# Kernel tuning notes

Hardware: AMD Instinct MI355X
Metric: run time of the kernel (lower is better)

The kernel has to match this reference:

```python
import jax, jax.numpy as jnp
import numpy as np

E = 4        # num_edge_types
C = 4        # num_channels (must equal E due to module's layer>0 einsum)
N = 2048     # num_nodes
W_IN = 256
W_OUT = 128


def _xavier_uniform(key, shape):
    # torch.nn.init.xavier_uniform_ on a 2D tensor [fan_out, fan_in] style
    fan_out, fan_in = shape[0], shape[1]
    bound = float(np.sqrt(6.0 / (fan_in + fan_out)))
    return jax.random.uniform(key, shape, jnp.float32, -bound, bound)


def setup_inputs() -> dict:
    key = jax.random.key(0)
    k = jax.random.split(key, 7)
    A = jax.random.uniform(k[0], (E, N, N), jnp.float32)   # non-negative dense multi-relation adjacency
    X = jax.random.normal(k[1], (N, W_IN), jnp.float32)
    gt_w1 = _xavier_uniform(k[2], (C, E))   # layer0 conv1
    gt_w2 = _xavier_uniform(k[3], (C, E))   # layer0 conv2
    gt_w3 = _xavier_uniform(k[4], (C, C))   # layer1 conv1 (C == E)
    gcn_w = _xavier_uniform(k[5], (W_IN, W_OUT))
    gcn_b = jnp.zeros((W_OUT,), jnp.float32)
    return {"A": A, "X": X, "gt_w1": gt_w1, "gt_w2": gt_w2, "gt_w3": gt_w3,
            "gcn_w": gcn_w, "gcn_b": gcn_b}


def _normalize_adj(adj):
    # adj: [N, N]. Symmetric degree normalization D^-1/2 (A+I) D^-1/2,
    # expressed as broadcasted row/col scaling (math-identical to the
    # original diag-matmul-matmul formulation).
    adj = adj + jnp.eye(adj.shape[0], dtype=adj.dtype)
    deg = adj.sum(axis=1)
    d = deg ** -0.5
    d = jnp.where(jnp.isinf(d), jnp.zeros_like(d), d)
    return d[:, None] * adj * d[None, :]


def reference(A, X, gt_w1, gt_w2, gt_w3, gcn_w, gcn_b):
    # --- GT layer 0 (first=True): two softmax-weighted mixes of A, then bmm ---
    fw1 = jax.nn.softmax(gt_w1, axis=1)
    fw2 = jax.nn.softmax(gt_w2, axis=1)
    Ha = jnp.einsum('oi,inm->onm', fw1, A)   # [C, N, N]
    Hb = jnp.einsum('oi,inm->onm', fw2, A)   # [C, N, N]
    H = jnp.matmul(Ha, Hb)                   # [C, N, N]
    # --- GT layer 1 (first=False): H @ (softmax mix of A) ---
    fw3 = jax.nn.softmax(gt_w3, axis=1)
    Hc = jnp.einsum('oi,inm->onm', fw3, A)   # [C, N, N]
    H = jnp.matmul(H, Hc)                    # [C, N, N]
    # --- per-channel degree-normalized GCN conv ---
    Hn = jax.vmap(_normalize_adj)(H)         # [C, N, N]
    support = X @ gcn_w                      # [N, W_OUT] (shared across channels)
    out = jnp.einsum('cnm,mf->cnf', Hn, support) + gcn_b  # [C, N, W_OUT]
    out = jax.nn.relu(out)
    # torch.cat(X_out, dim=1): channel blocks side by side -> [N, C*W_OUT]
    return jnp.transpose(out, (1, 0, 2)).reshape(N, C * W_OUT)
```

## Files before the change

kernel.cpp:

```cpp
#include <hip/hip_runtime.h>
#include <math.h>

#define N_NODES 2048
#define NNE ((long)N_NODES * N_NODES)

#define SUPD_SCALE 8192.0f

typedef _Float16 half4_t __attribute__((ext_vector_type(4)));
typedef _Float16 half8_t __attribute__((ext_vector_type(8)));
typedef float    floatx4 __attribute__((ext_vector_type(4)));

__device__ __forceinline__ void async_cp16(const void* g, void* l) {
  __builtin_amdgcn_global_load_lds((const __attribute__((address_space(1))) void*)g,
                                   (__attribute__((address_space(3))) void*)l,
                                   16, 0, 0);
}

__device__ __forceinline__ float colscale_from(float cn) {
  return exp2f((float)(10 - ilogbf(fmaxf(cn, 1e-37f))));
}

__global__ void softmax3_zero_k(const float* __restrict__ w1,
                                const float* __restrict__ w2,
                                const float* __restrict__ w3,
                                float* __restrict__ fw,
                                float* __restrict__ cn) {
  int t = threadIdx.x;
  float4 z4 = {0.f, 0.f, 0.f, 0.f};
  ((float4*)cn)[t] = z4;
  if (t < 12) {
    const float* src = (t < 4) ? w1 : (t < 8) ? w2 : w3;
    int r = t & 3;
    float v0 = src[r * 4 + 0], v1 = src[r * 4 + 1];
    float v2 = src[r * 4 + 2], v3 = src[r * 4 + 3];
    float m = fmaxf(fmaxf(v0, v1), fmaxf(v2, v3));
    float e0 = expf(v0 - m), e1 = expf(v1 - m), e2 = expf(v2 - m), e3 = expf(v3 - m);
    float inv = 1.0f / (e0 + e1 + e2 + e3);
    fw[t * 4 + 0] = e0 * inv; fw[t * 4 + 1] = e1 * inv;
    fw[t * 4 + 2] = e2 * inv; fw[t * 4 + 3] = e3 * inv;
  }
}

__global__ __launch_bounds__(128)
void support_k(const float* __restrict__ X, const float* __restrict__ W,
               float* __restrict__ sup) {
  __shared__ float Xs[256];
  const int t = threadIdx.x;
  const int m = blockIdx.x;
  Xs[t]       = X[(long)m * 256 + t];
  Xs[t + 128] = X[(long)m * 256 + t + 128];
  __syncthreads();
  float acc = 0.f;
  #pragma unroll 8
  for (int k = 0; k < 256; ++k) acc = fmaf(Xs[k], W[(long)k * 128 + t], acc);
  sup[(long)m * 128 + t] = acc;
}

__global__ __launch_bounds__(256)
void rc_from_A_k(const float* __restrict__ A, const float* __restrict__ fw,
                 float* __restrict__ rc) {
  __shared__ float red[4][4];
  const int r = blockIdx.x;
  const int w = threadIdx.x >> 6, lane = threadIdx.x & 63;
  float se[4];
  #pragma unroll
  for (int e = 0; e < 4; ++e) {
    const float4* row = (const float4*)(A + (long)e * NNE + (long)r * N_NODES);
    float s = 0.f;
    #pragma unroll
    for (int q = 0; q < 2; ++q) {
      float4 a = row[w * 128 + q * 64 + lane];
      s += (a.x + a.y) + (a.z + a.w);
    }
    se[e] = s;
  }
  float m[4];
  #pragma unroll
  for (int c = 0; c < 4; ++c)
    m[c] = fw[32 + c * 4 + 0] * se[0] + fw[32 + c * 4 + 1] * se[1] +
           fw[32 + c * 4 + 2] * se[2] + fw[32 + c * 4 + 3] * se[3];
  #pragma unroll
  for (int o = 32; o > 0; o >>= 1) {
    #pragma unroll
    for (int c = 0; c < 4; ++c) m[c] += __shfl_down(m[c], o, 64);
  }
  if (lane == 0) {
    #pragma unroll
    for (int c = 0; c < 4; ++c) red[w][c] = m[c];
  }
  __syncthreads();
  if (threadIdx.x < 4) {
    int c = threadIdx.x;
    rc[c * N_NODES + r] = (red[0][c] + red[1][c]) + (red[2][c] + red[3][c]);
  }
}

__global__ __launch_bounds__(256)
void matvecA_k(const float* __restrict__ A, const float* __restrict__ fw, int off,
               const float* __restrict__ vin, float* __restrict__ vout) {
  __shared__ float red[4][4];
  const int r = blockIdx.x;
  const int w = threadIdx.x >> 6, lane = threadIdx.x & 63;
  float acc[4][4] = {{0.f}};
  #pragma unroll
  for (int q = 0; q < 2; ++q) {
    const int j4 = w * 128 + q * 64 + lane;
    float4 v0 = *(const float4*)&vin[0 * 2048 + j4 * 4];
    float4 v1 = *(const float4*)&vin[1 * 2048 + j4 * 4];
    float4 v2 = *(const float4*)&vin[2 * 2048 + j4 * 4];
    float4 v3 = *(const float4*)&vin[3 * 2048 + j4 * 4];
    #pragma unroll
    for (int e = 0; e < 4; ++e) {
      float4 a = *(const float4*)(A + (long)e * NNE + (long)r * N_NODES + j4 * 4);
      acc[e][0] += (a.x * v0.x + a.y * v0.y) + (a.z * v0.z + a.w * v0.w);
      acc[e][1] += (a.x * v1.x + a.y * v1.y) + (a.z * v1.z + a.w * v1.w);
      acc[e][2] += (a.x * v2.x + a.y * v2.y) + (a.z * v2.z + a.w * v2.w);
      acc[e][3] += (a.x * v3.x + a.y * v3.y) + (a.z * v3.z + a.w * v3.w);
    }
  }
  float m[4];
  #pragma unroll
  for (int c = 0; c < 4; ++c)
    m[c] = fw[off + c * 4 + 0] * acc[0][c] + fw[off + c * 4 + 1] * acc[1][c] +
           fw[off + c * 4 + 2] * acc[2][c] + fw[off + c * 4 + 3] * acc[3][c];
  #pragma unroll
  for (int o = 32; o > 0; o >>= 1) {
    #pragma unroll
    for (int c = 0; c < 4; ++c) m[c] += __shfl_down(m[c], o, 64);
  }
  if (lane == 0) {
    #pragma unroll
    for (int c = 0; c < 4; ++c) red[w][c] = m[c];
  }
  __syncthreads();
  if (threadIdx.x < 4) {
    int c = threadIdx.x;
    vout[c * N_NODES + r] = (red[0][c] + red[1][c]) + (red[2][c] + red[3][c]);
  }
}

__global__ __launch_bounds__(256)
void transposeV_k(const float* __restrict__ sup, const float* __restrict__ deg,
                  float* __restrict__ dvec,
                  _Float16* __restrict__ TH, _Float16* __restrict__ TL,
                  float* __restrict__ cn0) {
  __shared__ _Float16 sh[32][33], sl[32][33];
  __shared__ float red[8][32];
  const int t = threadIdx.x;
  const int z = blockIdx.z;
  const int m0 = blockIdx.x * 32, f0 = blockIdx.y * 32;
  const int r0 = t >> 5, col = t & 31;
  float part = 0.f;
  #pragma unroll
  for (int m = 0; m < 4; ++m) {
    const int row = m0 + r0 + 8 * m;
    float dm = 1.0f / sqrtf(1.0f + deg[(long)z * N_NODES + row]);
    float sv = sup[(long)row * 128 + f0 + col] * dm;
    if (blockIdx.y == 0 && col == 0) dvec[(long)z * N_NODES + row] = dm;
    float v = sv * SUPD_SCALE;
    _Float16 h = (_Float16)v;
    sh[r0 + 8 * m][col] = h;
    sl[r0 + 8 * m][col] = (_Float16)(v - (float)h);
    part += fabsf(v);
  }
  red[r0][col] = part;
  __syncthreads();
  if (t < 32) {
    float s = 0.f;
    #pragma unroll
    for (int q = 0; q < 8; ++q) s += red[q][t];
    atomicAdd(&cn0[(long)z * 128 + f0 + t], s);
  }
  const int rr = t >> 3, cq = (t & 7) * 4;
  half4_t oh, ol;
  #pragma unroll
  for (int d = 0; d < 4; ++d) { oh[d] = sh[cq + d][rr]; ol[d] = sl[cq + d][rr]; }
  long ob = (long)z * 128 * N_NODES + (long)(f0 + rr) * N_NODES + m0 + cq;
  *(half4_t*)(TH + ob) = oh;
  *(half4_t*)(TL + ob) = ol;
}

__global__ __launch_bounds__(256, 2)
void gemm_mix_k(const float* __restrict__ A, const float* __restrict__ fw, int off,
                const _Float16* __restrict__ BH, const _Float16* __restrict__ BL,
                float* __restrict__ C) {
  __shared__ __align__(16) _Float16 BsArr[3 * 8192];
  __shared__ __align__(16) _Float16 HsArr[2 * 2048];

  const int t = threadIdx.x;
  const int lane = t & 63;
  const int w = t >> 6;
  const int bid = blockIdx.x;
  const int tile = bid & 63;
  const int ch = (bid >> 6) & 3;
  const int kc = bid >> 8;
  const int i0 = tile * 32;
  const long koff = (long)kc * 512;

  float wv[4];
  #pragma unroll
  for (int e = 0; e < 4; ++e) wv[e] = fw[off + ch * 4 + e];

  const int rr = t >> 3;
  const int k4 = (t & 7) * 4;
  const float* gA = A + (long)(i0 + rr) * N_NODES + koff + k4;
  const int hoff = rr * 32 + (((k4 >> 3) + (rr >> 1)) & 3) * 8 + (k4 & 7);

  const int hls = w >> 1;
  const int half = w & 1;
  const int kc_st = (((lane & 3) - ((lane >> 3) & 3)) & 3) * 8;
  const _Float16* gB = (hls ? BL : BH)
                     + ((long)ch * 128 + half * 64 + (lane >> 2)) * (long)N_NODES
                     + koff + kc_st;

  const int wm = w >> 1, wn = w & 1;
  const int fr = lane & 15;
  const int fq = lane >> 4;
  const int fkz = ((fq + (fr >> 1)) & 3) * 8;
  const int aoff = (wm * 16 + fr) * 32 + fkz;

  floatx4 acc[4];
  #pragma unroll
  for (int j = 0; j < 4; ++j) {
    floatx4 zz4 = {0.f, 0.f, 0.f, 0.f};
    acc[j] = zz4;
  }

  float4 sA[4], sB[4], sC[4];

  auto loadA = [&](float4* av, int kt) {
    const float* g = gA + kt * 32;
    av[0] = *(const float4*)(g);
    av[1] = *(const float4*)(g + NNE);
    av[2] = *(const float4*)(g + 2 * NNE);
    av[3] = *(const float4*)(g + 3 * NNE);
  };
  auto stageB = [&](int buf, int kt) {
    _Float16* lb = BsArr + buf * 8192 + hls * 4096 + half * 2048;
    const _Float16* g = gB + kt * 32;
    #pragma unroll
    for (int q = 0; q < 4; ++q)
      async_cp16(g + (long)q * (16L * N_NODES), lb + q * 512 + lane * 8);
  };
  auto mixStore = [&](const float4* av, int hb) {
    half4_t h, l;
    #pragma unroll
    for (int d = 0; d < 4; ++d) {
      float o = wv[0] * ((const float*)&av[0])[d] + wv[1] * ((const float*)&av[1])[d] +
                wv[2] * ((const float*)&av[2])[d] + wv[3] * ((const float*)&av[3])[d];
      _Float16 hh = (_Float16)o;
      h[d] = hh; l[d] = (_Float16)(o - (float)hh);
    }
    *(half4_t*)&HsArr[hb * 2048 + hoff] = h;
    *(half4_t*)&HsArr[hb * 2048 + 1024 + hoff] = l;
  };
  auto domfma = [&](int buf, int hb) {
    half8_t ah = *(const half8_t*)&HsArr[hb * 2048 + aoff];
    half8_t al = *(const half8_t*)&HsArr[hb * 2048 + 1024 + aoff];
    const _Float16* bb = BsArr + buf * 8192;
    #pragma unroll
    for (int nt = 0; nt < 4; ++nt) {
      const int bo = (wn * 64 + nt * 16 + fr) * 32 + fkz;
      half8_t bh = *(const half8_t*)&bb[bo];
      half8_t bl = *(const half8_t*)&bb[4096 + bo];
      acc[nt] = __builtin_amdgcn_mfma_f32_16x16x32_f16(ah, bh, acc[nt], 0, 0, 0);
      acc[nt] = __builtin_amdgcn_mfma_f32_16x16x32_f16(al, bh, acc[nt], 0, 0, 0);
      acc[nt] = __builtin_amdgcn_mfma_f32_16x16x32_f16(ah, bl, acc[nt], 0, 0, 0);
    }
  };

#define SB0 __builtin_amdgcn_sched_barrier(0)
#define BAR_V8  do { SB0; asm volatile("s_waitcnt vmcnt(8) lgkmcnt(0)" ::: "memory"); \
                     SB0; __builtin_amdgcn_s_barrier(); SB0; } while (0)
#define BAR_V4  do { SB0; asm volatile("s_waitcnt vmcnt(4) lgkmcnt(0)" ::: "memory"); \
                     SB0; __builtin_amdgcn_s_barrier(); SB0; } while (0)

#define SEGMENT(KT, PA, PM, BUFS, BUFM)                                       \
  do {                                                                        \
    if ((KT) + 3 < 16) loadA(PA, (KT) + 3);                                   \
    if ((KT) + 2 < 16) stageB(BUFS, (KT) + 2);                                \
    domfma(BUFM, (KT) & 1);                                                   \
    if ((KT) + 1 < 16) mixStore(PM, ((KT) + 1) & 1);                          \
    if ((KT) <= 12)      BAR_V8;                                              \
    else if ((KT) == 13) BAR_V4;                                              \
    else if ((KT) == 14) __syncthreads();                                     \
  } while (0)

  loadA(sA, 0); loadA(sB, 1); loadA(sC, 2);
  stageB(0, 0); stageB(1, 1);
  mixStore(sA, 0);
  BAR_V4;

  SEGMENT(0,  sA, sB, 2, 0);
  SEGMENT(1,  sB, sC, 0, 1);
  SEGMENT(2,  sC, sA, 1, 2);
  SEGMENT(3,  sA, sB, 2, 0);
  SEGMENT(4,  sB, sC, 0, 1);
  SEGMENT(5,  sC, sA, 1, 2);
  SEGMENT(6,  sA, sB, 2, 0);
  SEGMENT(7,  sB, sC, 0, 1);
  SEGMENT(8,  sC, sA, 1, 2);
  SEGMENT(9,  sA, sB, 2, 0);
  SEGMENT(10, sB, sC, 0, 1);
  SEGMENT(11, sC, sA, 1, 2);
  SEGMENT(12, sA, sB, 2, 0);
  SEGMENT(13, sB, sC, 0, 1);
  SEGMENT(14, sC, sA, 1, 2);
  SEGMENT(15, sA, sB, 2, 0);

#undef SEGMENT
#undef BAR_V8
#undef BAR_V4
#undef SB0

  const int er = fq * 4;
  const int ec = lane & 15;
  float* Cb = C + ((long)(kc * 4 + ch) * N_NODES + i0 + wm * 16) * 128;
  #pragma unroll
  for (int nt = 0; nt < 4; ++nt) {
    const int f = wn * 64 + nt * 16 + ec;
    #pragma unroll
    for (int r = 0; r < 4; ++r)
      Cb[(long)(er + r) * 128 + f] = acc[nt][r];
  }
}

__global__ __launch_bounds__(256)
void combineT_k(const float* __restrict__ P, int parts,
                const float* __restrict__ cn_in, float* __restrict__ cn_out,
                _Float16* __restrict__ TH, _Float16* __restrict__ TL) {
  __shared__ _Float16 sh[32][33], sl[32][33];
  __shared__ float red[8][32];
  const int t = threadIdx.x;
  const int z = blockIdx.z;
  const int j0 = blockIdx.x * 32, f0 = blockIdx.y * 32;
  const int r0 = t >> 5, col = t & 31;
  const float s = colscale_from(cn_in[(long)z * 128 + f0 + col]);
  const long step = 4L * N_NODES * 128;
  float part = 0.f;
  #pragma unroll
  for (int m = 0; m < 4; ++m) {
    long idx = ((long)z * N_NODES + j0 + r0 + 8 * m) * 128 + f0 + col;
    float v = (P[idx] + P[idx + step]) + (P[idx + 2 * step] + P[idx + 3 * step]);
    v *= s;
    _Float16 h = (_Float16)v;
    sh[r0 + 8 * m][col] = h;
    sl[r0 + 8 * m][col] = (_Float16)(v - (float)h);
    part += fabsf(v);
  }
  if (cn_out) red[r0][col] = part;
  __syncthreads();
  if (cn_out && t < 32) {
    float ss = 0.f;
    #pragma unroll
    for (int q = 0; q < 8; ++q) ss += red[q][t];
    atomicAdd(&cn_out[(long)z * 128 + f0 + t], ss);
  }
  const int rr = t >> 3, cq = (t & 7) * 4;
  half4_t oh, ol;
  #pragma unroll
  for (int d = 0; d < 4; ++d) { oh[d] = sh[cq + d][rr]; ol[d] = sl[cq + d][rr]; }
  long ob = (long)z * 128 * N_NODES + (long)(f0 + rr) * N_NODES + j0 + cq;
  *(half4_t*)(TH + ob) = oh;
  *(half4_t*)(TL + ob) = ol;
}

__global__ __launch_bounds__(256)
void final_k(const float4* __restrict__ T2, const float4* __restrict__ sup4,
             const float* __restrict__ dvec, const float* __restrict__ cn0,
             const float* __restrict__ cn1, const float* __restrict__ bias,
             float* __restrict__ out) {
  const int t = threadIdx.x;
  const int z = blockIdx.y;
  const int idx = blockIdx.x * 256 + t;
  const int i = idx >> 5;
  const int fq = (idx & 31) * 4;
  const long step4 = 4L * N_NODES * 32;
  long b4 = (long)z * N_NODES * 32 + idx;
  float4 s0 = T2[b4];
  float4 s1 = T2[b4 + step4];
  float4 s2 = T2[b4 + 2 * step4];
  float4 s3 = T2[b4 + 3 * step4];
  float4 su = sup4[idx];
  const float dn = dvec[(long)z * N_NODES + i];
  const float dn2 = dn * dn;
  float inv[4];
  #pragma unroll
  for (int d = 0; d < 4; ++d) {
    int i0 = ilogbf(fmaxf(cn0[(long)z * 128 + fq + d], 1e-37f));
    int i1 = ilogbf(fmaxf(cn1[(long)z * 128 + fq + d], 1e-37f));
    inv[d] = exp2f((float)(i0 + i1 - 33)) * dn;
  }
  float4 o;
  o.x = fmaxf(((s0.x + s1.x) + (s2.x + s3.x)) * inv[0] + dn2 * su.x + bias[fq + 0], 0.f);
  o.y = fmaxf(((s0.y + s1.y) + (s2.y + s3.y)) * inv[1] + dn2 * su.y + bias[fq + 1], 0.f);
  o.z = fmaxf(((s0.z + s1.z) + (s2.z + s3.z)) * inv[2] + dn2 * su.z + bias[fq + 2], 0.f);
  o.w = fmaxf(((s0.w + s1.w) + (s2.w + s3.w)) * inv[3] + dn2 * su.w + bias[fq + 3], 0.f);
  *(float4*)(out + (long)i * 512 + z * 128 + fq) = o;
}

extern "C" void kernel_launch(void* const* d_in, const int* in_sizes, int n_in,
                              void* d_out, int out_size, void* d_ws, size_t ws_size,
                              hipStream_t stream) {
  const float* A  = (const float*)d_in[0];
  const float* X  = (const float*)d_in[1];
  const float* w1 = (const float*)d_in[2];
  const float* w2 = (const float*)d_in[3];
  const float* w3 = (const float*)d_in[4];
  const float* gw = (const float*)d_in[5];
  const float* gb = (const float*)d_in[6];
  float* out = (float*)d_out;

  float* ws   = (float*)d_ws;
  float* fw   = ws;
  float* rc   = fw + 64;
  float* v1   = rc + 4 * N_NODES;
  float* deg  = v1 + 4 * N_NODES;
  float* dvec = deg + 4 * N_NODES;
  float* sup  = dvec + 4 * N_NODES;
  float* cn0  = sup + (long)N_NODES * 128;
  float* cn1  = cn0 + 512;
  float* Mtmp = cn1 + 512;
  _Float16* arena = (_Float16*)(Mtmp + 16L * N_NODES * 128);
  _Float16* VTH = arena;
  _Float16* VTL = VTH + 4L * 128 * N_NODES;
  _Float16* T0H = VTL + 4L * 128 * N_NODES;
  _Float16* T0L = T0H + 4L * 128 * N_NODES;
  _Float16* T1H = T0L + 4L * 128 * N_NODES;
  _Float16* T1L = T1H + 4L * 128 * N_NODES;

  softmax3_zero_k<<<1, 256, 0, stream>>>(w1, w2, w3, fw, cn0);
  support_k<<<N_NODES, 128, 0, stream>>>(X, gw, sup);
  rc_from_A_k<<<N_NODES, 256, 0, stream>>>(A, fw, rc);
  matvecA_k<<<N_NODES, 256, 0, stream>>>(A, fw, 16, rc, v1);
  matvecA_k<<<N_NODES, 256, 0, stream>>>(A, fw, 0, v1, deg);
  transposeV_k<<<dim3(64, 4, 4), 256, 0, stream>>>(sup, deg, dvec,
                                                   VTH, VTL, cn0);
  gemm_mix_k<<<1024, 256, 0, stream>>>(A, fw, 32, VTH, VTL, Mtmp);
  combineT_k<<<dim3(64, 4, 4), 256, 0, stream>>>(Mtmp, 4, cn0, cn1, T0H, T0L);
  gemm_mix_k<<<1024, 256, 0, stream>>>(A, fw, 16, T0H, T0L, Mtmp);
  combineT_k<<<dim3(64, 4, 4), 256, 0, stream>>>(Mtmp, 4, cn1, nullptr, T1H, T1L);
  gemm_mix_k<<<1024, 256, 0, stream>>>(A, fw, 0, T1H, T1L, Mtmp);
  final_k<<<dim3(256, 4), 256, 0, stream>>>((const float4*)Mtmp,
                                            (const float4*)sup, dvec,
                                            cn0, cn1, gb, out);
}
```

Measured before the change: 267.7 us.

## Compute two channels per gemm_mix block with 64-row tiles and reverse matvec order

gemm_mix_k now uses 512-thread blocks that cover 64 rows and two output channels at once. Each A tile loaded from global memory is mixed into two channel operands, so the fp32 A reads are amortised across channels and the block count drops from 1024 to 256. LDS use grows (B buffers doubled, H buffers quadrupled) and occupancy drops to one block per CU, which may reduce latency hiding. Separately, the first matvec runs its rows in reverse order, probably so it reuses A rows the previous kernel left in cache.

```diff
diff --git a/kernel.cpp b/kernel.cpp
--- a/kernel.cpp
+++ b/kernel.cpp
@@ -97,9 +97,9 @@
 
 __global__ __launch_bounds__(256)
 void matvecA_k(const float* __restrict__ A, const float* __restrict__ fw, int off,
-               const float* __restrict__ vin, float* __restrict__ vout) {
+               const float* __restrict__ vin, float* __restrict__ vout, int rev) {
   __shared__ float red[4][4];
-  const int r = blockIdx.x;
+  const int r = rev ? (N_NODES - 1 - blockIdx.x) : blockIdx.x;
   const int w = threadIdx.x >> 6, lane = threadIdx.x & 63;
   float acc[4][4] = {{0.f}};
   #pragma unroll
@@ -180,51 +180,58 @@
   *(half4_t*)(TL + ob) = ol;
 }
 
-__global__ __launch_bounds__(256, 2)
+__global__ __launch_bounds__(512, 1)
 void gemm_mix_k(const float* __restrict__ A, const float* __restrict__ fw, int off,
                 const _Float16* __restrict__ BH, const _Float16* __restrict__ BL,
                 float* __restrict__ C) {
-  __shared__ __align__(16) _Float16 BsArr[3 * 8192];
-  __shared__ __align__(16) _Float16 HsArr[2 * 2048];
+  __shared__ __align__(16) _Float16 BsArr[3 * 16384];
+  __shared__ __align__(16) _Float16 HsArr[2 * 8192];
 
   const int t = threadIdx.x;
   const int lane = t & 63;
   const int w = t >> 6;
   const int bid = blockIdx.x;
-  const int tile = bid & 63;
-  const int ch = (bid >> 6) & 3;
-  const int kc = bid >> 8;
-  const int i0 = tile * 32;
+  const int tile = bid & 31;
+  const int chp = (bid >> 5) & 1;
+  const int kc = bid >> 6;
+  const int i0 = tile * 64;
+  const int ch0 = chp * 2;
   const long koff = (long)kc * 512;
 
-  float wv[4];
-  #pragma unroll
-  for (int e = 0; e < 4; ++e) wv[e] = fw[off + ch * 4 + e];
+  float wv0[4], wv1[4];
+  #pragma unroll
+  for (int e = 0; e < 4; ++e) {
+    wv0[e] = fw[off + ch0 * 4 + e];
+    wv1[e] = fw[off + (ch0 + 1) * 4 + e];
+  }
 
   const int rr = t >> 3;
   const int k4 = (t & 7) * 4;
   const float* gA = A + (long)(i0 + rr) * N_NODES + koff + k4;
   const int hoff = rr * 32 + (((k4 >> 3) + (rr >> 1)) & 3) * 8 + (k4 & 7);
 
-  const int hls = w >> 1;
-  const int half = w & 1;
+  const int sch = w >> 2, spl = (w >> 1) & 1, shalf = w & 1;
   const int kc_st = (((lane & 3) - ((lane >> 3) & 3)) & 3) * 8;
-  const _Float16* gB = (hls ? BL : BH)
-                     + ((long)ch * 128 + half * 64 + (lane >> 2)) * (long)N_NODES
-                     + koff + kc_st;
-
-  const int wm = w >> 1, wn = w & 1;
+  const _Float16* gB = (spl ? BL : BH)
+      + ((long)(ch0 + sch) * 128 + shalf * 64 + (lane >> 2)) * (long)N_NODES
+      + koff + kc_st;
+  const int sdst = sch * 8192 + spl * 4096 + shalf * 2048;
+
+  const int wm = w >> 1;
+  const int wn = w & 1;
   const int fr = lane & 15;
   const int fq = lane >> 4;
   const int fkz = ((fq + (fr >> 1)) & 3) * 8;
   const int aoff = (wm * 16 + fr) * 32 + fkz;
 
-  floatx4 acc[4];
-  #pragma unroll
-  for (int j = 0; j < 4; ++j) {
-    floatx4 zz4 = {0.f, 0.f, 0.f, 0.f};
-    acc[j] = zz4;
-  }
+  floatx4 acc[2][4];
+  #pragma unroll
+  for (int c = 0; c < 2; ++c)
+    #pragma unroll
+    for (int j = 0; j < 4; ++j) {
+      floatx4 zz4 = {0.f, 0.f, 0.f, 0.f};
+      acc[c][j] = zz4;
+    }
 
   float4 sA[4], sB[4], sC[4];
 
@@ -236,36 +243,46 @@
     av[3] = *(const float4*)(g + 3 * NNE);
   };
   auto stageB = [&](int buf, int kt) {
-    _Float16* lb = BsArr + buf * 8192 + hls * 4096 + half * 2048;
+    _Float16* lb = BsArr + buf * 16384 + sdst;
     const _Float16* g = gB + kt * 32;
     #pragma unroll
     for (int q = 0; q < 4; ++q)
       async_cp16(g + (long)q * (16L * N_NODES), lb + q * 512 + lane * 8);
   };
   auto mixStore = [&](const float4* av, int hb) {
-    half4_t h, l;
+    half4_t h0, l0, h1, l1;
     #pragma unroll
     for (int d = 0; d < 4; ++d) {
-      float o = wv[0] * ((const float*)&av[0])[d] + wv[1] * ((const float*)&av[1])[d] +
-                wv[2] * ((const float*)&av[2])[d] + wv[3] * ((const float*)&av[3])[d];
-      _Float16 hh = (_Float16)o;
-      h[d] = hh; l[d] = (_Float16)(o - (float)hh);
-    }
-    *(half4_t*)&HsArr[hb * 2048 + hoff] = h;
-    *(half4_t*)&HsArr[hb * 2048 + 1024 + hoff] = l;
+      float a0 = ((const float*)&av[0])[d], a1 = ((const float*)&av[1])[d];
+      float a2 = ((const float*)&av[2])[d], a3 = ((const float*)&av[3])[d];
+      float o0 = wv0[0] * a0 + wv0[1] * a1 + wv0[2] * a2 + wv0[3] * a3;
+      float o1 = wv1[0] * a0 + wv1[1] * a1 + wv1[2] * a2 + wv1[3] * a3;
+      _Float16 hh0 = (_Float16)o0, hh1 = (_Float16)o1;
+      h0[d] = hh0; l0[d] = (_Float16)(o0 - (float)hh0);
+      h1[d] = hh1; l1[d] = (_Float16)(o1 - (float)hh1);
+    }
+    _Float16* hb0 = HsArr + hb * 8192;
+    *(half4_t*)&hb0[hoff] = h0;
+    *(half4_t*)&hb0[2048 + hoff] = l0;
+    *(half4_t*)&hb0[4096 + hoff] = h1;
+    *(half4_t*)&hb0[6144 + hoff] = l1;
   };
   auto domfma = [&](int buf, int hb) {
-    half8_t ah = *(const half8_t*)&HsArr[hb * 2048 + aoff];
-    half8_t al = *(const half8_t*)&HsArr[hb * 2048 + 1024 + aoff];
-    const _Float16* bb = BsArr + buf * 8192;
-    #pragma unroll
-    for (int nt = 0; nt < 4; ++nt) {
-      const int bo = (wn * 64 + nt * 16 + fr) * 32 + fkz;
-      half8_t bh = *(const half8_t*)&bb[bo];
-      half8_t bl = *(const half8_t*)&bb[4096 + bo];
-      acc[nt] = __builtin_amdgcn_mfma_f32_16x16x32_f16(ah, bh, acc[nt], 0, 0, 0);
-      acc[nt] = __builtin_amdgcn_mfma_f32_16x16x32_f16(al, bh, acc[nt], 0, 0, 0);
-      acc[nt] = __builtin_amdgcn_mfma_f32_16x16x32_f16(ah, bl, acc[nt], 0, 0, 0);
+    const _Float16* hbse = HsArr + hb * 8192;
+    const _Float16* bbse = BsArr + buf * 16384;
+    #pragma unroll
+    for (int c = 0; c < 2; ++c) {
+      half8_t ah = *(const half8_t*)&hbse[c * 4096 + aoff];
+      half8_t al = *(const half8_t*)&hbse[c * 4096 + 2048 + aoff];
+      #pragma unroll
+      for (int nt = 0; nt < 4; ++nt) {
+        const int bo = c * 8192 + (wn * 64 + nt * 16 + fr) * 32 + fkz;
+        half8_t bh = *(const half8_t*)&bbse[bo];
+        half8_t bl = *(const half8_t*)&bbse[bo + 4096];
+        acc[c][nt] = __builtin_amdgcn_mfma_f32_16x16x32_f16(ah, bh, acc[c][nt], 0, 0, 0);
+        acc[c][nt] = __builtin_amdgcn_mfma_f32_16x16x32_f16(al, bh, acc[c][nt], 0, 0, 0);
+        acc[c][nt] = __builtin_amdgcn_mfma_f32_16x16x32_f16(ah, bl, acc[c][nt], 0, 0, 0);
+      }
     }
   };
 
@@ -315,13 +332,16 @@
 
   const int er = fq * 4;
   const int ec = lane & 15;
-  float* Cb = C + ((long)(kc * 4 + ch) * N_NODES + i0 + wm * 16) * 128;
-  #pragma unroll
-  for (int nt = 0; nt < 4; ++nt) {
-    const int f = wn * 64 + nt * 16 + ec;
-    #pragma unroll
-    for (int r = 0; r < 4; ++r)
-      Cb[(long)(er + r) * 128 + f] = acc[nt][r];
+  #pragma unroll
+  for (int c = 0; c < 2; ++c) {
+    float* Cb = C + ((long)(kc * 4 + ch0 + c) * N_NODES + i0 + wm * 16) * 128;
+    #pragma unroll
+    for (int nt = 0; nt < 4; ++nt) {
+      const int f = wn * 64 + nt * 16 + ec;
+      #pragma unroll
+      for (int r = 0; r < 4; ++r)
+        Cb[(long)(er + r) * 128 + f] = acc[c][nt][r];
+    }
   }
 }
 
@@ -432,15 +452,15 @@
   softmax3_zero_k<<<1, 256, 0, stream>>>(w1, w2, w3, fw, cn0);
   support_k<<<N_NODES, 128, 0, stream>>>(X, gw, sup);
   rc_from_A_k<<<N_NODES, 256, 0, stream>>>(A, fw, rc);
-  matvecA_k<<<N_NODES, 256, 0, stream>>>(A, fw, 16, rc, v1);
-  matvecA_k<<<N_NODES, 256, 0, stream>>>(A, fw, 0, v1, deg);
+  matvecA_k<<<N_NODES, 256, 0, stream>>>(A, fw, 16, rc, v1, 1);
+  matvecA_k<<<N_NODES, 256, 0, stream>>>(A, fw, 0, v1, deg, 0);
   transposeV_k<<<dim3(64, 4, 4), 256, 0, stream>>>(sup, deg, dvec,
                                                    VTH, VTL, cn0);
-  gemm_mix_k<<<1024, 256, 0, stream>>>(A, fw, 32, VTH, VTL, Mtmp);
+  gemm_mix_k<<<256, 512, 0, stream>>>(A, fw, 32, VTH, VTL, Mtmp);
   combineT_k<<<dim3(64, 4, 4), 256, 0, stream>>>(Mtmp, 4, cn0, cn1, T0H, T0L);
-  gemm_mix_k<<<1024, 256, 0, stream>>>(A, fw, 16, T0H, T0L, Mtmp);
+  gemm_mix_k<<<256, 512, 0, stream>>>(A, fw, 16, T0H, T0L, Mtmp);
   combineT_k<<<dim3(64, 4, 4), 256, 0, stream>>>(Mtmp, 4, cn1, nullptr, T1H, T1L);
-  gemm_mix_k<<<1024, 256, 0, stream>>>(A, fw, 0, T1H, T1L, Mtmp);
+  gemm_mix_k<<<256, 512, 0, stream>>>(A, fw, 0, T1H, T1L, Mtmp);
   final_k<<<dim3(256, 4), 256, 0, stream>>>((const float4*)Mtmp,
                                             (const float4*)sup, dvec,
                                             cn0, cn1, gb, out);
```

After: 241.0 us. -10.0%, faster.
